# Kernel optimization log

Measured on AMD Instinct MI355X. Metric: run time of the kernel, lower is better.

The kernel has to match this reference:

```python
import jax, jax.numpy as jnp
import numpy as np

TEMPERATURE = 0.5
COS_EPS = 1e-8  # torch.nn.CosineSimilarity default eps


def setup_inputs() -> dict:
    key = jax.random.key(0)
    k1, k2 = jax.random.split(key)
    N, D = 4096, 128
    z_i = jax.random.normal(k1, (N, D), dtype=jnp.float32)
    z_j = jax.random.normal(k2, (N, D), dtype=jnp.float32)
    return {"z_i": z_i, "z_j": z_j}


def reference(z_i, z_j):
    t = TEMPERATURE
    # L2-normalize each row (torch.norm over dim=1, then divide)
    zi = z_i / jnp.linalg.norm(z_i, axis=1, keepdims=True)
    zj = z_j / jnp.linalg.norm(z_j, axis=1, keepdims=True)
    z_ij = jnp.concatenate([zi, zj], axis=0)  # [2N, D]
    z_ji = jnp.concatenate([zj, zi], axis=0)  # [2N, D]
    # Full pairwise similarity matrix, scaled by temperature: [2N, 2N]
    sim = jnp.matmul(z_ij, z_ij.T) / t
    exp_sim = jnp.exp(sim)
    exp_sum = jnp.sum(exp_sim, axis=1)          # row reduction
    diag = jnp.diagonal(exp_sim)                # self-similarity terms
    # numerator: exp(cosine_similarity(z_ij, z_ji) / t) — positive pairs
    cos = jnp.sum(z_ij * z_ji, axis=1) / jnp.maximum(
        jnp.linalg.norm(z_ij, axis=1) * jnp.linalg.norm(z_ji, axis=1), COS_EPS)
    numerator = jnp.exp(cos / t)
    denominator = exp_sum - diag
    loss = -jnp.log(numerator / denominator)
    return jnp.mean(loss)
```

## Files before the change

kernel.cpp:

```cpp
#include <hip/hip_runtime.h>
#include <hip/hip_bf16.h>

typedef __attribute__((ext_vector_type(2))) long vlong2;
typedef __attribute__((ext_vector_type(4))) float floatx4;

#define D_DIM 128
#define SCALE_F 1.6986436f
#define CS 16
#define CTILE 64
#define BLK_ROWS 256
#define MREP 4

typedef __attribute__((address_space(1))) const unsigned int GUI;
typedef __attribute__((address_space(3))) unsigned int LUI;
#define GLOAD16(g, l) __builtin_amdgcn_global_load_lds((GUI*)(g), (LUI*)(l), 16, 0, 0)

__global__ void prep_kernel(const float* __restrict__ zi,
                            const float* __restrict__ zj,
                            unsigned char* __restrict__ Z8,
                            float* __restrict__ posdot,
                            float* __restrict__ selfarg, int N) {
    int r = blockIdx.x * 4 + (threadIdx.x >> 6);
    int t = threadIdx.x & 63;
    const float* pi = zi + (size_t)r * D_DIM;
    const float* pj = zj + (size_t)r * D_DIM;
    float a0 = pi[2 * t], a1 = pi[2 * t + 1];
    float b0 = pj[2 * t], b1 = pj[2 * t + 1];
    float ssi = a0*a0 + a1*a1;
    float ssj = b0*b0 + b1*b1;
    float sij = a0*b0 + a1*b1;
#pragma unroll
    for (int off = 1; off < 64; off <<= 1) {
        ssi += __shfl_xor(ssi, off);
        ssj += __shfl_xor(ssj, off);
        sij += __shfl_xor(sij, off);
    }
    float ni = sqrtf(ssi), nj = sqrtf(ssj);
    float ri = SCALE_F / ni, rj = SCALE_F / nj;
    int ui = __builtin_amdgcn_cvt_pk_fp8_f32(a0 * ri, a1 * ri, 0, false);
    int uj = __builtin_amdgcn_cvt_pk_fp8_f32(b0 * rj, b1 * rj, 0, false);
    *(ushort*)&Z8[(size_t)r * D_DIM + 2 * t]       = (ushort)(ui & 0xffff);
    *(ushort*)&Z8[(size_t)(r + N) * D_DIM + 2 * t] = (ushort)(uj & 0xffff);
    float fi0 = __builtin_amdgcn_cvt_f32_fp8(ui, 0);
    float fi1 = __builtin_amdgcn_cvt_f32_fp8(ui, 1);
    float fj0 = __builtin_amdgcn_cvt_f32_fp8(uj, 0);
    float fj1 = __builtin_amdgcn_cvt_f32_fp8(uj, 1);
    float sdi = fi0*fi0 + fi1*fi1;
    float sdj = fj0*fj0 + fj1*fj1;
#pragma unroll
    for (int off = 1; off < 64; off <<= 1) {
        sdi += __shfl_xor(sdi, off);
        sdj += __shfl_xor(sdj, off);
    }
    if (t == 0) {
        posdot[r] = sij / fmaxf(ni * nj, 1e-8f);
        selfarg[r]     = sdi;
        selfarg[r + N] = sdj;
    }
}

__global__ __launch_bounds__(512, 4)
void main_kernel(const unsigned char* __restrict__ Z8,
                 float* __restrict__ rowpart, int N2) {
    __shared__ unsigned char Btile[2][CTILE * D_DIM];

    const int tid  = threadIdx.x;
    const int lane = tid & 63;
    const int wave = tid >> 6;
    const int mw   = wave & 3;
    const int nh   = wave >> 2;
    const int m    = lane & 15;
    const int kg   = lane >> 4;
    const int rwave0 = blockIdx.x * BLK_ROWS + mw * 64;
    const int cy   = blockIdx.y;

    const int cols_per_chunk = N2 / CS;
    const int ntile = cols_per_chunk / CTILE;
    const int c0base = cy * cols_per_chunk;

    const int scol = tid >> 3;
    const int sv   = (tid & 7) ^ (scol & 7);
    const unsigned char* gsrc = Z8 + (size_t)(c0base + scol) * D_DIM
                                   + (sv >> 1) * 32 + (sv & 1) * 16;
    const size_t tadv = (size_t)CTILE * D_DIM;

    GLOAD16(gsrc, &Btile[0][(size_t)tid * 16]);

    vlong2 afrag[MREP][2];
#pragma unroll
    for (int rb = 0; rb < MREP; ++rb) {
        const unsigned char* ap = Z8 + (size_t)(rwave0 + rb * 16 + m) * D_DIM + kg * 32;
        afrag[rb][0] = *(const vlong2*)(ap);
        afrag[rb][1] = *(const vlong2*)(ap + 16);
    }
#pragma unroll
    for (int rb = 0; rb < MREP; ++rb) {
        asm volatile("" : "+v"(afrag[rb][0]));
        asm volatile("" : "+v"(afrag[rb][1]));
    }

    float rowacc[MREP][4];
#pragma unroll
    for (int rb = 0; rb < MREP; ++rb)
#pragma unroll
        for (int g = 0; g < 4; ++g) rowacc[rb][g] = 0.0f;

    __syncthreads();

    for (int t = 0; t < ntile; ++t) {
        if (t + 1 < ntile)
            GLOAD16(gsrc + (size_t)(t + 1) * tadv,
                    &Btile[(t + 1) & 1][(size_t)tid * 16]);

        const unsigned char* buf = Btile[t & 1];
#pragma unroll
        for (int s2 = 0; s2 < 2; ++s2) {
            const int bcol = nh * 32 + s2 * 16 + m;
            const int cb   = bcol * D_DIM;
            vlong2 bq0 = *(const vlong2*)&buf[cb + (((kg * 2 + 0) ^ (bcol & 7)) * 16)];
            vlong2 bq1 = *(const vlong2*)&buf[cb + (((kg * 2 + 1) ^ (bcol & 7)) * 16)];
#pragma unroll
            for (int rb = 0; rb < MREP; ++rb) {
                floatx4 ac0 = {0.f, 0.f, 0.f, 0.f};
                floatx4 ac1 = {0.f, 0.f, 0.f, 0.f};
                ac0 = __builtin_amdgcn_mfma_f32_16x16x32_fp8_fp8(afrag[rb][0].x, bq0.x, ac0, 0, 0, 0);
                ac1 = __builtin_amdgcn_mfma_f32_16x16x32_fp8_fp8(afrag[rb][1].x, bq1.x, ac1, 0, 0, 0);
                ac0 = __builtin_amdgcn_mfma_f32_16x16x32_fp8_fp8(afrag[rb][0].y, bq0.y, ac0, 0, 0, 0);
                ac1 = __builtin_amdgcn_mfma_f32_16x16x32_fp8_fp8(afrag[rb][1].y, bq1.y, ac1, 0, 0, 0);
#pragma unroll
                for (int g = 0; g < 4; ++g)
                    rowacc[rb][g] += __builtin_amdgcn_exp2f(ac0[g] + ac1[g]);
            }
        }
        __syncthreads();
    }

#pragma unroll
    for (int rb = 0; rb < MREP; ++rb)
#pragma unroll
        for (int g = 0; g < 4; ++g) {
            float v = rowacc[rb][g];
            v += __shfl_xor(v, 1);
            v += __shfl_xor(v, 2);
            v += __shfl_xor(v, 4);
            v += __shfl_xor(v, 8);
            if (m == 0) {
                int grow = rwave0 + rb * 16 + kg * 4 + g;
                rowpart[(size_t)(cy * 2 + nh) * N2 + grow] = v;
            }
        }
}

__global__ void finalize1_kernel(const float* __restrict__ rowpart,
                                 const float* __restrict__ selfarg,
                                 const float* __restrict__ posdot,
                                 float* __restrict__ bpart, int N2, int NP) {
    __shared__ float red[4];
    int tid = threadIdx.x;
    int r = blockIdx.x * 256 + tid;
    float d0 = 0.f, d1 = 0.f, d2 = 0.f, d3 = 0.f;
#pragma unroll
    for (int q = 0; q < 2 * CS; q += 4) {
        d0 += rowpart[(size_t)(q + 0) * N2 + r];
        d1 += rowpart[(size_t)(q + 1) * N2 + r];
        d2 += rowpart[(size_t)(q + 2) * N2 + r];
        d3 += rowpart[(size_t)(q + 3) * N2 + r];
    }
    float denom = (d0 + d1) + (d2 + d3);
    denom -= __builtin_amdgcn_exp2f(selfarg[r]);
    float pos = posdot[r < NP ? r : r - NP];
    float v = logf(denom) - 2.0f * pos;
#pragma unroll
    for (int off = 1; off < 64; off <<= 1) v += __shfl_xor(v, off);
    if ((tid & 63) == 0) red[tid >> 6] = v;
    __syncthreads();
    if (tid == 0) bpart[blockIdx.x] = red[0] + red[1] + red[2] + red[3];
}

__global__ void finalize2_kernel(const float* __restrict__ bpart,
                                 float* __restrict__ out, int nb, int N2) {
    int t = threadIdx.x;
    float v = (t < nb) ? bpart[t] : 0.0f;
#pragma unroll
    for (int off = 1; off < 64; off <<= 1) v += __shfl_xor(v, off);
    if (t == 0) out[0] = v / (float)N2;
}

extern "C" void kernel_launch(void* const* d_in, const int* in_sizes, int n_in,
                              void* d_out, int out_size, void* d_ws, size_t ws_size,
                              hipStream_t stream) {
    const float* zi = (const float*)d_in[0];
    const float* zj = (const float*)d_in[1];
    const int N  = in_sizes[0] / D_DIM;
    const int N2 = 2 * N;

    char* w = (char*)d_ws;
    unsigned char* Z8 = (unsigned char*)w;
    size_t off = (size_t)N2 * D_DIM;
    float* posdot  = (float*)(w + off);  off += (size_t)N  * sizeof(float);
    float* selfarg = (float*)(w + off);  off += (size_t)N2 * sizeof(float);
    float* rowpart = (float*)(w + off);  off += (size_t)(2 * CS) * N2 * sizeof(float);
    float* bpart   = (float*)(w + off);

    prep_kernel<<<N / 4, 256, 0, stream>>>(zi, zj, Z8, posdot, selfarg, N);
    dim3 grid(N2 / BLK_ROWS, CS);
    main_kernel<<<grid, 512, 0, stream>>>(Z8, rowpart, N2);
    const int nb = N2 / 256;
    finalize1_kernel<<<nb, 256, 0, stream>>>(rowpart, selfarg, posdot, bpart, N2, N);
    finalize2_kernel<<<1, 64, 0, stream>>>(bpart, (float*)d_out, nb, N2);
}
```

Baseline: 32.03 us.

## Load whole column chunk into LDS once and drop per-tile double buffering

Replaces the double-buffered 64-column tile loop with a single upfront async load of the block's entire 512-column chunk into LDS, followed by a sync-free compute loop. This removes the eight per-tile barriers and the prefetch bookkeeping. In exchange, LDS use per block grows fourfold, which can cut resident blocks per CU, and the global-load latency is no longer hidden behind compute within a block.

```diff
diff --git a/kernel.cpp b/kernel.cpp
--- a/kernel.cpp
+++ b/kernel.cpp
@@ -7,7 +7,7 @@
 #define D_DIM 128
 #define SCALE_F 1.6986436f
 #define CS 16
-#define CTILE 64
+#define CCHUNK 512
 #define BLK_ROWS 256
 #define MREP 4
 
@@ -62,7 +62,7 @@
 __global__ __launch_bounds__(512, 4)
 void main_kernel(const unsigned char* __restrict__ Z8,
                  float* __restrict__ rowpart, int N2) {
-    __shared__ unsigned char Btile[2][CTILE * D_DIM];
+    __shared__ unsigned char Btile[CCHUNK * D_DIM];
 
     const int tid  = threadIdx.x;
     const int lane = tid & 63;
@@ -72,19 +72,17 @@
     const int m    = lane & 15;
     const int kg   = lane >> 4;
     const int rwave0 = blockIdx.x * BLK_ROWS + mw * 64;
-    const int cy   = blockIdx.y;
-
-    const int cols_per_chunk = N2 / CS;
-    const int ntile = cols_per_chunk / CTILE;
-    const int c0base = cy * cols_per_chunk;
-
-    const int scol = tid >> 3;
-    const int sv   = (tid & 7) ^ (scol & 7);
-    const unsigned char* gsrc = Z8 + (size_t)(c0base + scol) * D_DIM
-                                   + (sv >> 1) * 32 + (sv & 1) * 16;
-    const size_t tadv = (size_t)CTILE * D_DIM;
-
-    GLOAD16(gsrc, &Btile[0][(size_t)tid * 16]);
+    const int c0base = blockIdx.y * CCHUNK;
+
+#pragma unroll
+    for (int i = 0; i < 8; ++i) {
+        int c   = i * 512 + tid;
+        int col = c >> 3;
+        int v   = (c & 7) ^ (col & 7);
+        const unsigned char* g = Z8 + (size_t)(c0base + col) * D_DIM
+                                    + (v >> 1) * 32 + (v & 1) * 16;
+        GLOAD16(g, &Btile[(size_t)c * 16]);
+    }
 
     vlong2 afrag[MREP][2];
 #pragma unroll
@@ -107,32 +105,24 @@
 
     __syncthreads();
 
-    for (int t = 0; t < ntile; ++t) {
-        if (t + 1 < ntile)
-            GLOAD16(gsrc + (size_t)(t + 1) * tadv,
-                    &Btile[(t + 1) & 1][(size_t)tid * 16]);
-
-        const unsigned char* buf = Btile[t & 1];
-#pragma unroll
-        for (int s2 = 0; s2 < 2; ++s2) {
-            const int bcol = nh * 32 + s2 * 16 + m;
-            const int cb   = bcol * D_DIM;
-            vlong2 bq0 = *(const vlong2*)&buf[cb + (((kg * 2 + 0) ^ (bcol & 7)) * 16)];
-            vlong2 bq1 = *(const vlong2*)&buf[cb + (((kg * 2 + 1) ^ (bcol & 7)) * 16)];
-#pragma unroll
-            for (int rb = 0; rb < MREP; ++rb) {
-                floatx4 ac0 = {0.f, 0.f, 0.f, 0.f};
-                floatx4 ac1 = {0.f, 0.f, 0.f, 0.f};
-                ac0 = __builtin_amdgcn_mfma_f32_16x16x32_fp8_fp8(afrag[rb][0].x, bq0.x, ac0, 0, 0, 0);
-                ac1 = __builtin_amdgcn_mfma_f32_16x16x32_fp8_fp8(afrag[rb][1].x, bq1.x, ac1, 0, 0, 0);
-                ac0 = __builtin_amdgcn_mfma_f32_16x16x32_fp8_fp8(afrag[rb][0].y, bq0.y, ac0, 0, 0, 0);
-                ac1 = __builtin_amdgcn_mfma_f32_16x16x32_fp8_fp8(afrag[rb][1].y, bq1.y, ac1, 0, 0, 0);
-#pragma unroll
-                for (int g = 0; g < 4; ++g)
-                    rowacc[rb][g] += __builtin_amdgcn_exp2f(ac0[g] + ac1[g]);
-            }
+#pragma unroll 4
+    for (int u = 0; u < 16; ++u) {
+        const int bcol = (u >> 1) * 64 + nh * 32 + (u & 1) * 16 + m;
+        const int cb   = bcol * D_DIM;
+        vlong2 bq0 = *(const vlong2*)&Btile[cb + (((kg * 2 + 0) ^ (bcol & 7)) * 16)];
+        vlong2 bq1 = *(const vlong2*)&Btile[cb + (((kg * 2 + 1) ^ (bcol & 7)) * 16)];
+#pragma unroll
+        for (int rb = 0; rb < MREP; ++rb) {
+            floatx4 ac0 = {0.f, 0.f, 0.f, 0.f};
+            floatx4 ac1 = {0.f, 0.f, 0.f, 0.f};
+            ac0 = __builtin_amdgcn_mfma_f32_16x16x32_fp8_fp8(afrag[rb][0].x, bq0.x, ac0, 0, 0, 0);
+            ac1 = __builtin_amdgcn_mfma_f32_16x16x32_fp8_fp8(afrag[rb][1].x, bq1.x, ac1, 0, 0, 0);
+            ac0 = __builtin_amdgcn_mfma_f32_16x16x32_fp8_fp8(afrag[rb][0].y, bq0.y, ac0, 0, 0, 0);
+            ac1 = __builtin_amdgcn_mfma_f32_16x16x32_fp8_fp8(afrag[rb][1].y, bq1.y, ac1, 0, 0, 0);
+#pragma unroll
+            for (int g = 0; g < 4; ++g)
+                rowacc[rb][g] += __builtin_amdgcn_exp2f(ac0[g] + ac1[g]);
         }
-        __syncthreads();
     }
 
 #pragma unroll
@@ -146,7 +136,7 @@
             v += __shfl_xor(v, 8);
             if (m == 0) {
                 int grow = rwave0 + rb * 16 + kg * 4 + g;
-                rowpart[(size_t)(cy * 2 + nh) * N2 + grow] = v;
+                rowpart[(size_t)(blockIdx.y * 2 + nh) * N2 + grow] = v;
             }
         }
 }
```

New measurement: 32.14 us. About the same (+0.4%).

## Switch similarity GEMM to 32x32x64 scaled FP8 MFMA tiles

Applied to the files above, without the earlier changes.

Replaces the 16x16x32 FP8 MFMA sequence with the gfx950 scaled 32x32x64 f8f6f4 MFMA using unit scales, so each wave computes 32-row by 32-column tiles in two instructions per row block. Operand fragments, LDS read patterns and the output row mapping are reworked for the 32x32 layout, and the row reduction gains one more shuffle stage. The aim is fewer MFMA issues and LDS reads per tile. In exchange the accumulators are wider and register pressure rises, and the lane-to-K mapping must match the instruction's operand layout exactly.

```diff
diff --git a/kernel.cpp b/kernel.cpp
--- a/kernel.cpp
+++ b/kernel.cpp
@@ -1,15 +1,17 @@
 #include <hip/hip_runtime.h>
 #include <hip/hip_bf16.h>
 
-typedef __attribute__((ext_vector_type(2))) long vlong2;
-typedef __attribute__((ext_vector_type(4))) float floatx4;
+typedef __attribute__((ext_vector_type(4))) int int4v;
+typedef __attribute__((ext_vector_type(8))) int int8v;
+typedef __attribute__((ext_vector_type(16))) float floatx16;
 
 #define D_DIM 128
 #define SCALE_F 1.6986436f
 #define CS 16
 #define CTILE 64
 #define BLK_ROWS 256
-#define MREP 4
+#define MREP 2
+#define UNIT_SCALE 0x7F7F7F7F
 
 typedef __attribute__((address_space(1))) const unsigned int GUI;
 typedef __attribute__((address_space(3))) unsigned int LUI;
@@ -69,29 +71,26 @@
     const int wave = tid >> 6;
     const int mw   = wave & 3;
     const int nh   = wave >> 2;
-    const int m    = lane & 15;
-    const int kg   = lane >> 4;
+    const int c32  = lane & 31;
+    const int h    = lane >> 5;
     const int rwave0 = blockIdx.x * BLK_ROWS + mw * 64;
-    const int cy   = blockIdx.y;
-
-    const int cols_per_chunk = N2 / CS;
-    const int ntile = cols_per_chunk / CTILE;
-    const int c0base = cy * cols_per_chunk;
+    const int c0base = blockIdx.y * (N2 / CS);
+
+    const int ntile = (N2 / CS) / CTILE;
 
     const int scol = tid >> 3;
-    const int sv   = (tid & 7) ^ (scol & 7);
-    const unsigned char* gsrc = Z8 + (size_t)(c0base + scol) * D_DIM
-                                   + (sv >> 1) * 32 + (sv & 1) * 16;
+    const int ssl  = (tid & 7) ^ (scol & 7);
+    const unsigned char* gsrc = Z8 + (size_t)(c0base + scol) * D_DIM + ssl * 16;
     const size_t tadv = (size_t)CTILE * D_DIM;
 
     GLOAD16(gsrc, &Btile[0][(size_t)tid * 16]);
 
-    vlong2 afrag[MREP][2];
+    int8v afrag[MREP][2];
 #pragma unroll
     for (int rb = 0; rb < MREP; ++rb) {
-        const unsigned char* ap = Z8 + (size_t)(rwave0 + rb * 16 + m) * D_DIM + kg * 32;
-        afrag[rb][0] = *(const vlong2*)(ap);
-        afrag[rb][1] = *(const vlong2*)(ap + 16);
+        const unsigned char* ap = Z8 + (size_t)(rwave0 + rb * 32 + c32) * D_DIM + h * 32;
+        afrag[rb][0] = *(const int8v*)(ap);
+        afrag[rb][1] = *(const int8v*)(ap + 64);
     }
 #pragma unroll
     for (int rb = 0; rb < MREP; ++rb) {
@@ -99,11 +98,10 @@
         asm volatile("" : "+v"(afrag[rb][1]));
     }
 
-    float rowacc[MREP][4];
+    floatx16 rowacc[MREP];
 #pragma unroll
     for (int rb = 0; rb < MREP; ++rb)
-#pragma unroll
-        for (int g = 0; g < 4; ++g) rowacc[rb][g] = 0.0f;
+        rowacc[rb] = (floatx16)0.0f;
 
     __syncthreads();
 
@@ -113,24 +111,26 @@
                     &Btile[(t + 1) & 1][(size_t)tid * 16]);
 
         const unsigned char* buf = Btile[t & 1];
-#pragma unroll
-        for (int s2 = 0; s2 < 2; ++s2) {
-            const int bcol = nh * 32 + s2 * 16 + m;
-            const int cb   = bcol * D_DIM;
-            vlong2 bq0 = *(const vlong2*)&buf[cb + (((kg * 2 + 0) ^ (bcol & 7)) * 16)];
-            vlong2 bq1 = *(const vlong2*)&buf[cb + (((kg * 2 + 1) ^ (bcol & 7)) * 16)];
-#pragma unroll
-            for (int rb = 0; rb < MREP; ++rb) {
-                floatx4 ac0 = {0.f, 0.f, 0.f, 0.f};
-                floatx4 ac1 = {0.f, 0.f, 0.f, 0.f};
-                ac0 = __builtin_amdgcn_mfma_f32_16x16x32_fp8_fp8(afrag[rb][0].x, bq0.x, ac0, 0, 0, 0);
-                ac1 = __builtin_amdgcn_mfma_f32_16x16x32_fp8_fp8(afrag[rb][1].x, bq1.x, ac1, 0, 0, 0);
-                ac0 = __builtin_amdgcn_mfma_f32_16x16x32_fp8_fp8(afrag[rb][0].y, bq0.y, ac0, 0, 0, 0);
-                ac1 = __builtin_amdgcn_mfma_f32_16x16x32_fp8_fp8(afrag[rb][1].y, bq1.y, ac1, 0, 0, 0);
-#pragma unroll
-                for (int g = 0; g < 4; ++g)
-                    rowacc[rb][g] += __builtin_amdgcn_exp2f(ac0[g] + ac1[g]);
-            }
+        const int bcol = nh * 32 + c32;
+        const int cb   = bcol * D_DIM;
+        const int c7   = bcol & 7;
+        int4v l00 = *(const int4v*)&buf[cb + (((h * 2 + 0) ^ c7) * 16)];
+        int4v l01 = *(const int4v*)&buf[cb + (((h * 2 + 1) ^ c7) * 16)];
+        int4v l10 = *(const int4v*)&buf[cb + (((4 + h * 2 + 0) ^ c7) * 16)];
+        int4v l11 = *(const int4v*)&buf[cb + (((4 + h * 2 + 1) ^ c7) * 16)];
+        int8v b0 = {l00[0], l00[1], l00[2], l00[3], l01[0], l01[1], l01[2], l01[3]};
+        int8v b1 = {l10[0], l10[1], l10[2], l10[3], l11[0], l11[1], l11[2], l11[3]};
+
+#pragma unroll
+        for (int rb = 0; rb < MREP; ++rb) {
+            floatx16 acc = (floatx16)0.0f;
+            acc = __builtin_amdgcn_mfma_scale_f32_32x32x64_f8f6f4(
+                      afrag[rb][0], b0, acc, 0, 0, 0, UNIT_SCALE, 0, UNIT_SCALE);
+            acc = __builtin_amdgcn_mfma_scale_f32_32x32x64_f8f6f4(
+                      afrag[rb][1], b1, acc, 0, 0, 0, UNIT_SCALE, 0, UNIT_SCALE);
+#pragma unroll
+            for (int g = 0; g < 16; ++g)
+                rowacc[rb][g] += __builtin_amdgcn_exp2f(acc[g]);
         }
         __syncthreads();
     }
@@ -138,15 +138,16 @@
 #pragma unroll
     for (int rb = 0; rb < MREP; ++rb)
 #pragma unroll
-        for (int g = 0; g < 4; ++g) {
+        for (int g = 0; g < 16; ++g) {
             float v = rowacc[rb][g];
             v += __shfl_xor(v, 1);
             v += __shfl_xor(v, 2);
             v += __shfl_xor(v, 4);
             v += __shfl_xor(v, 8);
-            if (m == 0) {
-                int grow = rwave0 + rb * 16 + kg * 4 + g;
-                rowpart[(size_t)(cy * 2 + nh) * N2 + grow] = v;
+            v += __shfl_xor(v, 16);
+            if (c32 == 0) {
+                int grow = rwave0 + rb * 32 + (g & 3) + 8 * (g >> 2) + 4 * h;
+                rowpart[(size_t)(blockIdx.y * 2 + nh) * N2 + grow] = v;
             }
         }
 }
```

New measurement: 32.55 us. No clear change (+1.6%).
